# Kernel optimization log

Hardware: AMD Instinct MI355X
Metric: run time of the kernel (lower is better)

Reference implementation:

```python
import jax, jax.numpy as jnp
import numpy as np

B, C, D, H, W = 2, 64, 8, 32, 32  # identity f/g mappings => intermediate_channels == input_channels == 64


def setup_inputs() -> dict:
    key = jax.random.key(0)
    k1, k2 = jax.random.split(key)
    x = jax.random.normal(k1, (B, C, D, H, W), dtype=jnp.float32)
    # w_mapping: 1x1 conv, intermediate_channels -> input_channels (here 64 -> 64)
    w_weight = jax.random.normal(k2, (C, C), dtype=jnp.float32) * (1.0 / np.sqrt(C))
    w_bias = jnp.zeros((C,), dtype=jnp.float32)
    return {"x": x, "w_weight": w_weight, "w_bias": w_bias}


def reference(x, w_weight, w_bias):
    b, c = x.shape[0], x.shape[1]
    spatial = x.shape[2:]
    n = int(np.prod(spatial))
    # f/g mappings are identity -> q, k, v are all the flattened input
    x_flat = x.reshape(b, c, n)              # [B, C, N]
    q = jnp.transpose(x_flat, (0, 2, 1))     # [B, N, C] (f_mapping_i, permuted)
    k = x_flat                               # [B, C, N] (f_mapping_j)
    v = jnp.transpose(x_flat, (0, 2, 1))     # [B, N, C] (g_x, permuted)
    f = jnp.einsum('bic,bcj->bij', q, k)     # [B, N, N] dot-product similarity
    f_norm = jax.nn.softmax(f, axis=-1)
    y = jnp.einsum('bij,bjc->bic', f_norm, v)  # [B, N, C]
    y = jnp.transpose(y, (0, 2, 1)).reshape(b, c, *spatial)  # [B, C, D, H, W]
    # w_mapping: 1x1 conv (pointwise linear over channels) + bias
    w_y = jnp.einsum('bc...,oc->bo...', y, w_weight) + w_bias.reshape((1, c) + (1,) * len(spatial))
    z = w_y + x  # residual
    return z
```

## Files before the change

kernel.cpp:

```cpp
#include <hip/hip_runtime.h>
#include <hip/hip_bf16.h>


constexpr int NC = 64;
constexpr int NN = 8192;
constexpr int NKV = 128;

typedef __attribute__((ext_vector_type(8))) short bf16x8;
typedef __attribute__((ext_vector_type(4))) float f32x4;

static __device__ __forceinline__ short f2bf(float f) {
    union { float f; unsigned u; } v; v.f = f;
    unsigned r = v.u + 0x7FFFu + ((v.u >> 16) & 1u);
    return (short)(r >> 16);
}
static __device__ __forceinline__ float bf2f(short h) {
    union { unsigned u; float f; } v;
    v.u = ((unsigned)(unsigned short)h) << 16;
    return v.f;
}

__global__ __launch_bounds__(256) void prep_kernel(
    const float* __restrict__ x, short* __restrict__ Xjc, short* __restrict__ Xcj)
{
    __shared__ short T[64 * 64];
    const int tid = threadIdx.x;
    const int jt = blockIdx.x;
    const int b  = blockIdx.y;
    const int bo = b * NC * NN;
    const int sc = tid >> 2, sq = tid & 3;

    const float* xr = x + bo + sc * NN + jt * 64 + sq * 16;
    float fl[16];
    *(float4*)&fl[0]  = *(const float4*)(xr + 0);
    *(float4*)&fl[4]  = *(const float4*)(xr + 4);
    *(float4*)&fl[8]  = *(const float4*)(xr + 8);
    *(float4*)&fl[12] = *(const float4*)(xr + 12);
    short h[16];
    #pragma unroll
    for (int e = 0; e < 16; ++e) h[e] = f2bf(fl[e]);

    bf16x8 v0, v1;
    #pragma unroll
    for (int e = 0; e < 8; ++e) { v0[e] = h[e]; v1[e] = h[8 + e]; }
    *(bf16x8*)&Xcj[bo + sc * NN + jt * 64 + sq * 16]     = v0;
    *(bf16x8*)&Xcj[bo + sc * NN + jt * 64 + sq * 16 + 8] = v1;

    #pragma unroll
    for (int jj = 0; jj < 16; ++jj) {
        int j = sq * 16 + jj;
        T[(j * 64 + sc) ^ ((j & 7) << 3)] = h[jj];
    }
    __syncthreads();

    const int jr = tid >> 2, cq = tid & 3;
    bf16x8 a0 = *(const bf16x8*)&T[(jr * 64 + cq * 16) ^ ((jr & 7) << 3)];
    bf16x8 a1 = *(const bf16x8*)&T[(jr * 64 + cq * 16 + 8) ^ ((jr & 7) << 3)];
    *(bf16x8*)&Xjc[bo + (jt * 64 + jr) * 64 + cq * 16]     = a0;
    *(bf16x8*)&Xjc[bo + (jt * 64 + jr) * 64 + cq * 16 + 8] = a1;
}

__global__ __launch_bounds__(256) void attn_fd_kernel(
    const short* __restrict__ Xjc, const short* __restrict__ Xcj,
    float* __restrict__ ypart, float* __restrict__ lpart, int tps)
{
    __shared__ short Pl[4][32 * 64];

    const int tid  = threadIdx.x;
    const int lane = tid & 63;
    const int wv   = tid >> 6;
    const int lo   = lane & 15;
    const int hi   = lane >> 4;

    const int b  = blockIdx.y;
    const int sp = blockIdx.z;
    const int bo = b * NC * NN;
    const int qbase = blockIdx.x * 128 + wv * 32;
    short* Pw = Pl[wv];

    bf16x8 qf[2][2];
    #pragma unroll
    for (int qs = 0; qs < 2; ++qs)
        #pragma unroll
        for (int kk = 0; kk < 2; ++kk)
            qf[qs][kk] = *(const bf16x8*)&Xjc[bo + (qbase + qs * 16 + lo) * 64 + kk * 32 + hi * 8];

    float mrow[2][4];
    #pragma unroll
    for (int qs = 0; qs < 2; ++qs) {
        float v = 0.0f;
        #pragma unroll
        for (int kk = 0; kk < 2; ++kk)
            #pragma unroll
            for (int e = 0; e < 8; ++e) { float q = bf2f(qf[qs][kk][e]); v += q * q; }
        v += __shfl_xor(v, 16);
        v += __shfl_xor(v, 32);
        #pragma unroll
        for (int r = 0; r < 4; ++r) mrow[qs][r] = __shfl(v, hi * 4 + r);
    }

    f32x4 acc[2][4];
    f32x4 lacc[2];
    #pragma unroll
    for (int qs = 0; qs < 2; ++qs) {
        #pragma unroll
        for (int ct = 0; ct < 4; ++ct)
            #pragma unroll
            for (int r = 0; r < 4; ++r) acc[qs][ct][r] = 0.0f;
        #pragma unroll
        for (int r = 0; r < 4; ++r) lacc[qs][r] = 0.0f;
    }
    bf16x8 ones;
    #pragma unroll
    for (int e = 0; e < 8; ++e) ones[e] = (short)0x3F80;

    const int jb0 = sp * tps, jb1 = jb0 + tps;
    bf16x8 kfc[4][2], kfn[4][2];
    #pragma unroll
    for (int jt = 0; jt < 4; ++jt)
        #pragma unroll
        for (int kk = 0; kk < 2; ++kk)
            kfc[jt][kk] = *(const bf16x8*)&Xjc[bo + (jb0 * 64 + jt * 16 + lo) * 64 + kk * 32 + hi * 8];

    for (int jb = jb0; jb < jb1; ++jb) {
        bf16x8 vf[4][2];
        #pragma unroll
        for (int ct = 0; ct < 4; ++ct)
            #pragma unroll
            for (int kk = 0; kk < 2; ++kk)
                vf[ct][kk] = *(const bf16x8*)&Xcj[bo + (ct * 16 + lo) * NN + jb * 64 + kk * 32 + hi * 8];
        const bool more = (jb + 1 < jb1);
        if (more) {
            #pragma unroll
            for (int jt = 0; jt < 4; ++jt)
                #pragma unroll
                for (int kk = 0; kk < 2; ++kk)
                    kfn[jt][kk] = *(const bf16x8*)&Xjc[bo + ((jb + 1) * 64 + jt * 16 + lo) * 64 + kk * 32 + hi * 8];
        }

        f32x4 s[2][4];
        #pragma unroll
        for (int qs = 0; qs < 2; ++qs)
            #pragma unroll
            for (int jt = 0; jt < 4; ++jt) {
                #pragma unroll
                for (int r = 0; r < 4; ++r) s[qs][jt][r] = 0.0f;
                #pragma unroll
                for (int kk = 0; kk < 2; ++kk)
                    s[qs][jt] = __builtin_amdgcn_mfma_f32_16x16x32_bf16(qf[qs][kk], kfc[jt][kk], s[qs][jt], 0, 0, 0);
            }

        #pragma unroll
        for (int qs = 0; qs < 2; ++qs)
            #pragma unroll
            for (int jt = 0; jt < 4; ++jt)
                #pragma unroll
                for (int r = 0; r < 4; ++r) {
                    float p = __expf(s[qs][jt][r] - mrow[qs][r]);
                    int i = qs * 16 + hi * 4 + r;
                    Pw[(i * 64 + jt * 16 + lo) ^ ((i & 7) << 3)] = f2bf(p);
                }
        asm volatile("s_waitcnt lgkmcnt(0)" ::: "memory");
        __builtin_amdgcn_sched_barrier(0);

        bf16x8 pf[2][2];
        #pragma unroll
        for (int qs = 0; qs < 2; ++qs)
            #pragma unroll
            for (int kk = 0; kk < 2; ++kk) {
                int row = qs * 16 + lo;
                pf[qs][kk] = *(const bf16x8*)&Pw[(row * 64 + kk * 32 + hi * 8) ^ ((row & 7) << 3)];
            }

        #pragma unroll
        for (int qs = 0; qs < 2; ++qs)
            #pragma unroll
            for (int kk = 0; kk < 2; ++kk)
                lacc[qs] = __builtin_amdgcn_mfma_f32_16x16x32_bf16(ones, pf[qs][kk], lacc[qs], 0, 0, 0);

        #pragma unroll
        for (int qs = 0; qs < 2; ++qs)
            #pragma unroll
            for (int ct = 0; ct < 4; ++ct)
                #pragma unroll
                for (int kk = 0; kk < 2; ++kk)
                    acc[qs][ct] = __builtin_amdgcn_mfma_f32_16x16x32_bf16(vf[ct][kk], pf[qs][kk], acc[qs][ct], 0, 0, 0);

        if (more) {
            #pragma unroll
            for (int jt = 0; jt < 4; ++jt)
                #pragma unroll
                for (int kk = 0; kk < 2; ++kk)
                    kfc[jt][kk] = kfn[jt][kk];
        }
    }

    float* yp = ypart + (size_t)(sp * 2 + b) * NC * NN;
    #pragma unroll
    for (int qs = 0; qs < 2; ++qs)
        #pragma unroll
        for (int ct = 0; ct < 4; ++ct)
            #pragma unroll
            for (int r = 0; r < 4; ++r) {
                int c = ct * 16 + hi * 4 + r;
                yp[c * NN + qbase + qs * 16 + lo] = acc[qs][ct][r];
            }
    if (hi == 0) {
        #pragma unroll
        for (int qs = 0; qs < 2; ++qs)
            lpart[(sp * 2 + b) * NN + qbase + qs * 16 + lo] = lacc[qs][0];
    }
}

__global__ __launch_bounds__(256) void combine_kernel(
    const float* __restrict__ x, const float* __restrict__ wmat,
    const float* __restrict__ wbias, const float* __restrict__ ypart,
    const float* __restrict__ lpart, float* __restrict__ out, int nsplit)
{
    const int tid  = threadIdx.x;
    const int lane = tid & 63;
    const int wv   = tid >> 6;
    const int lo   = lane & 15;
    const int hi   = lane >> 4;

    const int batch = blockIdx.y;
    const int b_off = batch * NC * NN;
    const int qwave = blockIdx.x * 64 + wv * 16;
    const int i     = qwave + lo;

    float L = 0.0f;
    for (int s = 0; s < nsplit; ++s) L += lpart[(s * 2 + batch) * NN + i];
    const float linv = 1.0f / L;

    float accm[4][4];
    #pragma unroll
    for (int ct = 0; ct < 4; ++ct)
        #pragma unroll
        for (int r = 0; r < 4; ++r) accm[ct][r] = 0.0f;
    for (int s = 0; s < nsplit; ++s) {
        const float* yp = ypart + (size_t)(s * 2 + batch) * NC * NN;
        #pragma unroll
        for (int ct = 0; ct < 4; ++ct)
            #pragma unroll
            for (int r = 0; r < 4; ++r) {
                int c = ct * 16 + hi * 4 + r;
                accm[ct][r] += yp[c * NN + qwave + lo];
            }
    }

    bf16x8 yf[2];
    #pragma unroll
    for (int kk = 0; kk < 2; ++kk)
        #pragma unroll
        for (int e = 0; e < 8; ++e)
            yf[kk][e] = f2bf(accm[kk * 2 + (e >> 2)][e & 3] * linv);

    f32x4 z[4];
    #pragma unroll
    for (int ot = 0; ot < 4; ++ot) {
        #pragma unroll
        for (int r = 0; r < 4; ++r) z[ot][r] = 0.0f;
        int o = ot * 16 + lo;
        #pragma unroll
        for (int kk = 0; kk < 2; ++kk) {
            float4 wa = *(const float4*)&wmat[o * 64 + kk * 32 + hi * 4];
            float4 wb = *(const float4*)&wmat[o * 64 + kk * 32 + 16 + hi * 4];
            bf16x8 wf;
            wf[0] = f2bf(wa.x); wf[1] = f2bf(wa.y); wf[2] = f2bf(wa.z); wf[3] = f2bf(wa.w);
            wf[4] = f2bf(wb.x); wf[5] = f2bf(wb.y); wf[6] = f2bf(wb.z); wf[7] = f2bf(wb.w);
            z[ot] = __builtin_amdgcn_mfma_f32_16x16x32_bf16(wf, yf[kk], z[ot], 0, 0, 0);
        }
    }

    #pragma unroll
    for (int ot = 0; ot < 4; ++ot)
        #pragma unroll
        for (int r = 0; r < 4; ++r) {
            int o = ot * 16 + hi * 4 + r;
            int idx = b_off + o * NN + qwave + lo;
            out[idx] = z[ot][r] + wbias[o] + x[idx];
        }
}

__global__ __launch_bounds__(256) void attn_nl_kernel(
    const float* __restrict__ x, const float* __restrict__ wmat,
    const float* __restrict__ wbias, float* __restrict__ out)
{
    __shared__ short Xcj[64 * 64];
    __shared__ short Xjc[64 * 64];
    __shared__ short Plds[4][16 * 64];

    const int tid  = threadIdx.x;
    const int lane = tid & 63;
    const int wv   = tid >> 6;
    const int lo   = lane & 15;
    const int hi   = lane >> 4;

    const int batch = blockIdx.y;
    const int b_off = batch * NC * NN;
    const int qwave = blockIdx.x * 64 + wv * 16;
    const int qrow  = qwave + lo;

    bf16x8 qf[2];
    #pragma unroll
    for (int kk = 0; kk < 2; ++kk)
        #pragma unroll
        for (int e = 0; e < 8; ++e) {
            int c = kk * 32 + hi * 8 + e;
            qf[kk][e] = f2bf(x[b_off + c * NN + qrow]);
        }

    f32x4 acc[4];
    #pragma unroll
    for (int ct = 0; ct < 4; ++ct)
        #pragma unroll
        for (int r = 0; r < 4; ++r) acc[ct][r] = 0.0f;
    float mrow[4], lrow[4];
    #pragma unroll
    for (int r = 0; r < 4; ++r) { mrow[r] = -INFINITY; lrow[r] = 0.0f; }

    const int sc = tid >> 2;
    const int sq = tid & 3;
    const float* xrow = x + b_off + sc * NN + sq * 16;

    for (int jb = 0; jb < NKV; ++jb) {
        const int jbase = jb * 64;
        __syncthreads();

        float fl[16];
        *(float4*)&fl[0]  = *(const float4*)(xrow + jbase + 0);
        *(float4*)&fl[4]  = *(const float4*)(xrow + jbase + 4);
        *(float4*)&fl[8]  = *(const float4*)(xrow + jbase + 8);
        *(float4*)&fl[12] = *(const float4*)(xrow + jbase + 12);
        short h[16];
        #pragma unroll
        for (int e = 0; e < 16; ++e) h[e] = f2bf(fl[e]);

        {
            bf16x8 v0, v1;
            #pragma unroll
            for (int e = 0; e < 8; ++e) { v0[e] = h[e]; v1[e] = h[8 + e]; }
            int base = sc * 64 + sq * 16;
            int sw = (sc & 7) << 3;
            *(bf16x8*)&Xcj[(base) ^ sw]     = v0;
            *(bf16x8*)&Xcj[(base + 8) ^ sw] = v1;
        }
        #pragma unroll
        for (int jj = 0; jj < 16; ++jj) {
            int j = sq * 16 + jj;
            Xjc[(j * 64 + sc) ^ ((j & 7) << 3)] = h[jj];
        }
        __syncthreads();

        f32x4 s[4];
        #pragma unroll
        for (int jt = 0; jt < 4; ++jt) {
            #pragma unroll
            for (int r = 0; r < 4; ++r) s[jt][r] = 0.0f;
            int j = jt * 16 + lo;
            #pragma unroll
            for (int kk = 0; kk < 2; ++kk) {
                bf16x8 kf = *(const bf16x8*)&Xjc[(j * 64 + kk * 32 + hi * 8) ^ ((j & 7) << 3)];
                s[jt] = __builtin_amdgcn_mfma_f32_16x16x32_bf16(qf[kk], kf, s[jt], 0, 0, 0);
            }
        }

        float tm[4];
        #pragma unroll
        for (int r = 0; r < 4; ++r)
            tm[r] = fmaxf(fmaxf(s[0][r], s[1][r]), fmaxf(s[2][r], s[3][r]));
        #pragma unroll
        for (int d = 1; d < 16; d <<= 1)
            #pragma unroll
            for (int r = 0; r < 4; ++r)
                tm[r] = fmaxf(tm[r], __shfl_xor(tm[r], d));

        float scl4[4];
        #pragma unroll
        for (int r = 0; r < 4; ++r) {
            float mnew = fmaxf(mrow[r], tm[r]);
            scl4[r] = __expf(mrow[r] - mnew);
            mrow[r] = mnew;
        }

        float rs[4] = {0.f, 0.f, 0.f, 0.f};
        #pragma unroll
        for (int jt = 0; jt < 4; ++jt)
            #pragma unroll
            for (int r = 0; r < 4; ++r) {
                float p = __expf(s[jt][r] - mrow[r]);
                rs[r] += p;
                int i = hi * 4 + r;
                Plds[wv][(i * 64 + jt * 16 + lo) ^ ((i & 7) << 3)] = f2bf(p);
            }
        #pragma unroll
        for (int d = 1; d < 16; d <<= 1)
            #pragma unroll
            for (int r = 0; r < 4; ++r)
                rs[r] += __shfl_xor(rs[r], d);
        #pragma unroll
        for (int r = 0; r < 4; ++r)
            lrow[r] = lrow[r] * scl4[r] + rs[r];

        {
            int srcl = (lo >> 2) << 4;
            float b0 = __shfl(scl4[0], srcl), b1 = __shfl(scl4[1], srcl);
            float b2 = __shfl(scl4[2], srcl), b3 = __shfl(scl4[3], srcl);
            int rr = lo & 3;
            float scl = rr == 0 ? b0 : rr == 1 ? b1 : rr == 2 ? b2 : b3;
            #pragma unroll
            for (int ct = 0; ct < 4; ++ct)
                #pragma unroll
                for (int r = 0; r < 4; ++r) acc[ct][r] *= scl;
        }

        asm volatile("s_waitcnt lgkmcnt(0)" ::: "memory");

        bf16x8 pf[2];
        #pragma unroll
        for (int kk = 0; kk < 2; ++kk)
            pf[kk] = *(const bf16x8*)&Plds[wv][(lo * 64 + kk * 32 + hi * 8) ^ ((lo & 7) << 3)];
        #pragma unroll
        for (int ct = 0; ct < 4; ++ct) {
            int c = ct * 16 + lo;
            #pragma unroll
            for (int kk = 0; kk < 2; ++kk) {
                bf16x8 vf = *(const bf16x8*)&Xcj[(c * 64 + kk * 32 + hi * 8) ^ ((c & 7) << 3)];
                acc[ct] = __builtin_amdgcn_mfma_f32_16x16x32_bf16(vf, pf[kk], acc[ct], 0, 0, 0);
            }
        }
    }

    float linv;
    {
        int srcl = (lo >> 2) << 4;
        float c0 = __shfl(lrow[0], srcl), c1 = __shfl(lrow[1], srcl);
        float c2 = __shfl(lrow[2], srcl), c3 = __shfl(lrow[3], srcl);
        int rr = lo & 3;
        float li = rr == 0 ? c0 : rr == 1 ? c1 : rr == 2 ? c2 : c3;
        linv = 1.0f / li;
    }

    bf16x8 yf[2];
    #pragma unroll
    for (int kk = 0; kk < 2; ++kk)
        #pragma unroll
        for (int e = 0; e < 8; ++e)
            yf[kk][e] = f2bf(acc[kk * 2 + (e >> 2)][e & 3] * linv);

    f32x4 z[4];
    #pragma unroll
    for (int ot = 0; ot < 4; ++ot) {
        #pragma unroll
        for (int r = 0; r < 4; ++r) z[ot][r] = 0.0f;
        int o = ot * 16 + lo;
        #pragma unroll
        for (int kk = 0; kk < 2; ++kk) {
            float4 wa = *(const float4*)&wmat[o * 64 + kk * 32 + hi * 4];
            float4 wb = *(const float4*)&wmat[o * 64 + kk * 32 + 16 + hi * 4];
            bf16x8 wf;
            wf[0] = f2bf(wa.x); wf[1] = f2bf(wa.y); wf[2] = f2bf(wa.z); wf[3] = f2bf(wa.w);
            wf[4] = f2bf(wb.x); wf[5] = f2bf(wb.y); wf[6] = f2bf(wb.z); wf[7] = f2bf(wb.w);
            z[ot] = __builtin_amdgcn_mfma_f32_16x16x32_bf16(wf, yf[kk], z[ot], 0, 0, 0);
        }
    }

    #pragma unroll
    for (int ot = 0; ot < 4; ++ot)
        #pragma unroll
        for (int r = 0; r < 4; ++r) {
            int o = ot * 16 + hi * 4 + r;
            int idx = b_off + o * NN + qwave + lo;
            out[idx] = z[ot][r] + wbias[o] + x[idx];
        }
}

extern "C" void kernel_launch(void* const* d_in, const int* in_sizes, int n_in,
                              void* d_out, int out_size, void* d_ws, size_t ws_size,
                              hipStream_t stream) {
    const float* x  = (const float*)d_in[0];
    const float* w  = (const float*)d_in[1];
    const float* b  = (const float*)d_in[2];
    float* out = (float*)d_out;

    const size_t xhalf = (size_t)2 * NC * NN;
    auto need = [&](int ns) -> size_t {
        return xhalf * 2 * sizeof(short)
             + (size_t)ns * 2 * NC * NN * sizeof(float)
             + (size_t)ns * 2 * NN * sizeof(float);
    };

    int ns = 0;
    if      (ws_size >= need(4)) ns = 4;
    else if (ws_size >= need(2)) ns = 2;
    else if (ws_size >= need(1)) ns = 1;

    if (ns) {
        short* Xjc = (short*)d_ws;
        short* Xcj = Xjc + xhalf;
        float* ypart = (float*)(Xcj + xhalf);
        float* lpart = ypart + (size_t)ns * 2 * NC * NN;
        const int tps = NKV / ns;
        prep_kernel<<<dim3(NKV, 2), 256, 0, stream>>>(x, Xjc, Xcj);
        attn_fd_kernel<<<dim3(NN / 128, 2, ns), 256, 0, stream>>>(Xjc, Xcj, ypart, lpart, tps);
        combine_kernel<<<dim3(NN / 64, 2), 256, 0, stream>>>(x, w, b, ypart, lpart, out, ns);
    } else {
        attn_nl_kernel<<<dim3(NN / 64, 2), 256, 0, stream>>>(x, w, b, out);
    }
}
```

Measured before the change: 190.5 us.

## Halve queries per wave in flash-decode attention to raise occupancy

Each wave now handles 16 query rows instead of 32, so the grid doubles and each wave needs fewer accumulator registers and half the LDS for P. Launch bounds ask for 4 blocks per CU, and s_setprio brackets the MFMA sections so waves interleave better. The explicit lgkmcnt wait before reading P back is removed. In exchange, K and V tiles are reloaded from global/L2 twice as often per query, which raises memory traffic.

```diff
diff --git a/kernel.cpp b/kernel.cpp
--- a/kernel.cpp
+++ b/kernel.cpp
@@ -60,11 +60,11 @@
     *(bf16x8*)&Xjc[bo + (jt * 64 + jr) * 64 + cq * 16 + 8] = a1;
 }
 
-__global__ __launch_bounds__(256) void attn_fd_kernel(
+__global__ __launch_bounds__(256, 4) void attn_fd_kernel(
     const short* __restrict__ Xjc, const short* __restrict__ Xcj,
     float* __restrict__ ypart, float* __restrict__ lpart, int tps)
 {
-    __shared__ short Pl[4][32 * 64];
+    __shared__ short Pl[4][16 * 64];
 
     const int tid  = threadIdx.x;
     const int lane = tid & 63;
@@ -75,41 +75,35 @@
     const int b  = blockIdx.y;
     const int sp = blockIdx.z;
     const int bo = b * NC * NN;
-    const int qbase = blockIdx.x * 128 + wv * 32;
+    const int qbase = blockIdx.x * 64 + wv * 16;
     short* Pw = Pl[wv];
 
-    bf16x8 qf[2][2];
-    #pragma unroll
-    for (int qs = 0; qs < 2; ++qs)
+    bf16x8 qf[2];
+    #pragma unroll
+    for (int kk = 0; kk < 2; ++kk)
+        qf[kk] = *(const bf16x8*)&Xjc[bo + (qbase + lo) * 64 + kk * 32 + hi * 8];
+
+    float mrow[4];
+    {
+        float v = 0.0f;
         #pragma unroll
         for (int kk = 0; kk < 2; ++kk)
-            qf[qs][kk] = *(const bf16x8*)&Xjc[bo + (qbase + qs * 16 + lo) * 64 + kk * 32 + hi * 8];
-
-    float mrow[2][4];
-    #pragma unroll
-    for (int qs = 0; qs < 2; ++qs) {
-        float v = 0.0f;
-        #pragma unroll
-        for (int kk = 0; kk < 2; ++kk)
-            #pragma unroll
-            for (int e = 0; e < 8; ++e) { float q = bf2f(qf[qs][kk][e]); v += q * q; }
+            #pragma unroll
+            for (int e = 0; e < 8; ++e) { float q = bf2f(qf[kk][e]); v += q * q; }
         v += __shfl_xor(v, 16);
         v += __shfl_xor(v, 32);
         #pragma unroll
-        for (int r = 0; r < 4; ++r) mrow[qs][r] = __shfl(v, hi * 4 + r);
-    }
-
-    f32x4 acc[2][4];
-    f32x4 lacc[2];
-    #pragma unroll
-    for (int qs = 0; qs < 2; ++qs) {
-        #pragma unroll
-        for (int ct = 0; ct < 4; ++ct)
-            #pragma unroll
-            for (int r = 0; r < 4; ++r) acc[qs][ct][r] = 0.0f;
-        #pragma unroll
-        for (int r = 0; r < 4; ++r) lacc[qs][r] = 0.0f;
-    }
+        for (int r = 0; r < 4; ++r) mrow[r] = __shfl(v, hi * 4 + r);
+    }
+
+    f32x4 acc[4];
+    f32x4 lacc;
+    #pragma unroll
+    for (int ct = 0; ct < 4; ++ct)
+        #pragma unroll
+        for (int r = 0; r < 4; ++r) acc[ct][r] = 0.0f;
+    #pragma unroll
+    for (int r = 0; r < 4; ++r) lacc[r] = 0.0f;
     bf16x8 ones;
     #pragma unroll
     for (int e = 0; e < 8; ++e) ones[e] = (short)0x3F80;
@@ -138,53 +132,43 @@
                     kfn[jt][kk] = *(const bf16x8*)&Xjc[bo + ((jb + 1) * 64 + jt * 16 + lo) * 64 + kk * 32 + hi * 8];
         }
 
-        f32x4 s[2][4];
-        #pragma unroll
-        for (int qs = 0; qs < 2; ++qs)
-            #pragma unroll
-            for (int jt = 0; jt < 4; ++jt) {
-                #pragma unroll
-                for (int r = 0; r < 4; ++r) s[qs][jt][r] = 0.0f;
-                #pragma unroll
-                for (int kk = 0; kk < 2; ++kk)
-                    s[qs][jt] = __builtin_amdgcn_mfma_f32_16x16x32_bf16(qf[qs][kk], kfc[jt][kk], s[qs][jt], 0, 0, 0);
+        f32x4 s[4];
+        __builtin_amdgcn_s_setprio(1);
+        #pragma unroll
+        for (int jt = 0; jt < 4; ++jt) {
+            #pragma unroll
+            for (int r = 0; r < 4; ++r) s[jt][r] = 0.0f;
+            #pragma unroll
+            for (int kk = 0; kk < 2; ++kk)
+                s[jt] = __builtin_amdgcn_mfma_f32_16x16x32_bf16(qf[kk], kfc[jt][kk], s[jt], 0, 0, 0);
+        }
+        __builtin_amdgcn_s_setprio(0);
+
+        #pragma unroll
+        for (int jt = 0; jt < 4; ++jt)
+            #pragma unroll
+            for (int r = 0; r < 4; ++r) {
+                float p = __expf(s[jt][r] - mrow[r]);
+                int i = hi * 4 + r;
+                Pw[(i * 64 + jt * 16 + lo) ^ ((i & 7) << 3)] = f2bf(p);
             }
 
-        #pragma unroll
-        for (int qs = 0; qs < 2; ++qs)
-            #pragma unroll
-            for (int jt = 0; jt < 4; ++jt)
-                #pragma unroll
-                for (int r = 0; r < 4; ++r) {
-                    float p = __expf(s[qs][jt][r] - mrow[qs][r]);
-                    int i = qs * 16 + hi * 4 + r;
-                    Pw[(i * 64 + jt * 16 + lo) ^ ((i & 7) << 3)] = f2bf(p);
-                }
-        asm volatile("s_waitcnt lgkmcnt(0)" ::: "memory");
-        __builtin_amdgcn_sched_barrier(0);
-
-        bf16x8 pf[2][2];
-        #pragma unroll
-        for (int qs = 0; qs < 2; ++qs)
-            #pragma unroll
-            for (int kk = 0; kk < 2; ++kk) {
-                int row = qs * 16 + lo;
-                pf[qs][kk] = *(const bf16x8*)&Pw[(row * 64 + kk * 32 + hi * 8) ^ ((row & 7) << 3)];
-            }
-
-        #pragma unroll
-        for (int qs = 0; qs < 2; ++qs)
+        bf16x8 pf[2];
+        #pragma unroll
+        for (int kk = 0; kk < 2; ++kk)
+            pf[kk] = *(const bf16x8*)&Pw[(lo * 64 + kk * 32 + hi * 8) ^ ((lo & 7) << 3)];
+
+        __builtin_amdgcn_s_setprio(1);
+        #pragma unroll
+        for (int kk = 0; kk < 2; ++kk)
+            lacc = __builtin_amdgcn_mfma_f32_16x16x32_bf16(ones, pf[kk], lacc, 0, 0, 0);
+
+        #pragma unroll
+        for (int ct = 0; ct < 4; ++ct)
             #pragma unroll
             for (int kk = 0; kk < 2; ++kk)
-                lacc[qs] = __builtin_amdgcn_mfma_f32_16x16x32_bf16(ones, pf[qs][kk], lacc[qs], 0, 0, 0);
-
-        #pragma unroll
-        for (int qs = 0; qs < 2; ++qs)
-            #pragma unroll
-            for (int ct = 0; ct < 4; ++ct)
-                #pragma unroll
-                for (int kk = 0; kk < 2; ++kk)
-                    acc[qs][ct] = __builtin_amdgcn_mfma_f32_16x16x32_bf16(vf[ct][kk], pf[qs][kk], acc[qs][ct], 0, 0, 0);
+                acc[ct] = __builtin_amdgcn_mfma_f32_16x16x32_bf16(vf[ct][kk], pf[kk], acc[ct], 0, 0, 0);
+        __builtin_amdgcn_s_setprio(0);
 
         if (more) {
             #pragma unroll
@@ -197,19 +181,14 @@
 
     float* yp = ypart + (size_t)(sp * 2 + b) * NC * NN;
     #pragma unroll
-    for (int qs = 0; qs < 2; ++qs)
-        #pragma unroll
-        for (int ct = 0; ct < 4; ++ct)
-            #pragma unroll
-            for (int r = 0; r < 4; ++r) {
-                int c = ct * 16 + hi * 4 + r;
-                yp[c * NN + qbase + qs * 16 + lo] = acc[qs][ct][r];
-            }
-    if (hi == 0) {
-        #pragma unroll
-        for (int qs = 0; qs < 2; ++qs)
-            lpart[(sp * 2 + b) * NN + qbase + qs * 16 + lo] = lacc[qs][0];
-    }
+    for (int ct = 0; ct < 4; ++ct)
+        #pragma unroll
+        for (int r = 0; r < 4; ++r) {
+            int c = ct * 16 + hi * 4 + r;
+            yp[c * NN + qbase + lo] = acc[ct][r];
+        }
+    if (hi == 0)
+        lpart[(sp * 2 + b) * NN + qbase + lo] = lacc[0];
 }
 
 __global__ __launch_bounds__(256) void combine_kernel(
@@ -502,7 +481,7 @@
         float* lpart = ypart + (size_t)ns * 2 * NC * NN;
         const int tps = NKV / ns;
         prep_kernel<<<dim3(NKV, 2), 256, 0, stream>>>(x, Xjc, Xcj);
-        attn_fd_kernel<<<dim3(NN / 128, 2, ns), 256, 0, stream>>>(Xjc, Xcj, ypart, lpart, tps);
+        attn_fd_kernel<<<dim3(NN / 64, 2, ns), 256, 0, stream>>>(Xjc, Xcj, ypart, lpart, tps);
         combine_kernel<<<dim3(NN / 64, 2), 256, 0, stream>>>(x, w, b, ypart, lpart, out, ns);
     } else {
         attn_nl_kernel<<<dim3(NN / 64, 2), 256, 0, stream>>>(x, w, b, out);
```

After: 358.6 us. 88.2% more time.
